# Kernel optimization log

Measured on AMD Instinct MI355X. Metric: run time of the kernel, lower is better.

Reference implementation:

```python
import jax, jax.numpy as jnp
import numpy as np

N, DIN, D, K, H, N_ITERS = 16384, 256, 1024, 64, 2048, 3
THRESH = 0.3
EPS = 1e-8


def layernorm(x):
    mu = jnp.mean(x, axis=-1, keepdims=True)
    var = jnp.var(x, axis=-1, keepdims=True)
    return (x - mu) * jax.lax.rsqrt(var + 1e-5)


def setup_inputs() -> dict:
    key = jax.random.key(0)
    ks = jax.random.split(key, 20)
    s = 0.02
    return {
        "detections_t": jax.random.normal(ks[0], (N, DIN), jnp.float32),
        "detections_t1": jax.random.normal(ks[1], (N, DIN), jnp.float32),
        "W_enc": s * jax.random.normal(ks[2], (DIN, D), jnp.float32),
        "b_enc": jnp.zeros((D,), jnp.float32),
        "Wq": s * jax.random.normal(ks[3], (D, D), jnp.float32),
        "bq": jnp.zeros((D,), jnp.float32),
        "Wk": s * jax.random.normal(ks[4], (D, D), jnp.float32),
        "bk": jnp.zeros((D,), jnp.float32),
        "Wv": s * jax.random.normal(ks[5], (D, D), jnp.float32),
        "bv": jnp.zeros((D,), jnp.float32),
        "Wi": s * jax.random.normal(ks[6], (3 * D, D), jnp.float32),  # GRU input weights
        "Wh": s * jax.random.normal(ks[7], (3 * D, D), jnp.float32),  # GRU hidden weights
        "bi": jnp.zeros((3 * D,), jnp.float32),
        "bh": jnp.zeros((3 * D,), jnp.float32),
        "W1": s * jax.random.normal(ks[8], (D, H), jnp.float32),
        "b1": jnp.zeros((H,), jnp.float32),
        "W2": s * jax.random.normal(ks[9], (H, D), jnp.float32),
        "b2": jnp.zeros((D,), jnp.float32),
        "slots_mu": s * jax.random.normal(ks[10], (1, D), jnp.float32),
        "init_noise": jax.random.normal(ks[11], (K, D), jnp.float32) * s,
    }


def _gru(u, h, Wi, Wh, bi, bh):
    gi = u @ Wi.T + bi          # [K, 3D]
    gh = h @ Wh.T + bh
    ir, iz, inn = jnp.split(gi, 3, axis=-1)
    hr, hz, hn = jnp.split(gh, 3, axis=-1)
    r = jax.nn.sigmoid(ir + hr)
    z = jax.nn.sigmoid(iz + hz)
    n = jnp.tanh(inn + r * hn)
    return (1.0 - z) * n + z * h


def _process_frame(dets, prev_slots, p):
    x = layernorm(dets @ p["W_enc"] + p["b_enc"])          # [N, D]
    k = x @ p["Wk"] + p["bk"]                               # [N, D]
    v = x @ p["Wv"] + p["bv"]                               # [N, D]
    slots = prev_slots if prev_slots is not None else p["slots_mu"] + p["init_noise"]
    scale = D ** -0.5
    for _ in range(N_ITERS):
        slots_prev = slots
        q = layernorm(slots) @ p["Wq"] + p["bq"]            # [K, D]
        dots = (q @ k.T) * scale                             # [K, N]
        attn = jax.nn.softmax(dots, axis=0)                  # slots compete per detection
        attn = attn / (jnp.sum(attn, axis=-1, keepdims=True) + EPS)
        updates = attn @ v                                   # [K, D]
        slots = _gru(updates, slots_prev, p["Wi"], p["Wh"], p["bi"], p["bh"])
        slots = slots + (jax.nn.relu(layernorm(slots) @ p["W1"] + p["b1"]) @ p["W2"] + p["b2"])
    return slots


def _slot_similarity(a, b):
    an = a / (jnp.linalg.norm(a, axis=-1, keepdims=True) + EPS)
    bn = b / (jnp.linalg.norm(b, axis=-1, keepdims=True) + EPS)
    return an @ bn.T                                         # [K, K]


def _greedy_match(sim):
    max_sims = jnp.max(sim, axis=1)
    max_idxs = jnp.argmax(sim, axis=1)
    order = jnp.argsort(-max_sims)
    def step(carry, idx):
        matches, used = carry
        j = max_idxs[idx]
        ok = jnp.logical_and(~used[j], max_sims[idx] > THRESH)
        matches = matches.at[idx].set(jnp.where(ok, j, matches[idx]))
        used = used.at[j].set(used[j] | ok)
        return (matches, used), None
    init = (jnp.full((K,), -1, jnp.int32), jnp.zeros((K,), jnp.bool_))
    (matches, _), _ = jax.lax.scan(step, init, order)
    return matches


def reference(detections_t, detections_t1, W_enc, b_enc, Wq, bq, Wk, bk, Wv, bv,
              Wi, Wh, bi, bh, W1, b1, W2, b2, slots_mu, init_noise):
    p = dict(W_enc=W_enc, b_enc=b_enc, Wq=Wq, bq=bq, Wk=Wk, bk=bk, Wv=Wv, bv=bv,
             Wi=Wi, Wh=Wh, bi=bi, bh=bh, W1=W1, b1=b1, W2=W2, b2=b2,
             slots_mu=slots_mu, init_noise=init_noise)
    prev_slots = _process_frame(detections_t, None, p)
    curr_slots = _process_frame(detections_t1, prev_slots, p)
    sim = _slot_similarity(prev_slots, curr_slots)
    matches = _greedy_match(sim)
    return matches, sim
```

## Files before the change

kernel.cpp:

```cpp
#include <hip/hip_runtime.h>
#include <hip/hip_bf16.h>
#include <type_traits>

typedef __hip_bfloat16 bf16;
typedef __attribute__((ext_vector_type(8))) short s16x8;
typedef __attribute__((ext_vector_type(4))) float f32x4;

#define N_DET 16384
#define DIN   256
#define DD    1024
#define KSLOT 64
#define HH    2048
#define TD    3072

__device__ __forceinline__ float b2f(bf16 x){ return __bfloat162float(x); }
__device__ __forceinline__ bf16  f2b(float x){ return __float2bfloat16(x); }
__device__ __forceinline__ float bits2f(short u){ return __uint_as_float(((unsigned)(unsigned short)u) << 16); }

__device__ __forceinline__ void gload_lds16(const void* g, void* l) {
  __builtin_amdgcn_global_load_lds(
      (const __attribute__((address_space(1))) unsigned int*)g,
      (__attribute__((address_space(3))) unsigned int*)l, 16, 0, 0);
}

__device__ __forceinline__ void big_compute(bf16* As, bf16* Bs,
    const bf16* __restrict__ Ap, const bf16* __restrict__ Bp, int K, f32x4 acc[4][4])
{
  const int tid = threadIdx.x;
  const int lane = tid & 63, wave = tid >> 6;
  const int wr = wave >> 1, wc = wave & 1;
  const int l15 = lane & 15, h = lane >> 4;
  const int rr = tid >> 3;
  const int qs = ((tid & 7) ^ (rr & 7)) * 8;

#pragma unroll
  for (int m = 0; m < 4; ++m)
#pragma unroll
    for (int n = 0; n < 4; ++n) acc[m][n] = {0.f, 0.f, 0.f, 0.f};

  for (int k0 = 0; k0 < K; k0 += 64) {
    __syncthreads();
#pragma unroll
    for (int g = 0; g < 4; ++g)
      gload_lds16(Ap + (size_t)(g * 32 + rr) * K + k0 + qs,
                  As + ((size_t)g * 256 + wave * 64) * 8);
#pragma unroll
    for (int g = 0; g < 4; ++g)
      gload_lds16(Bp + (size_t)(g * 32 + rr) * K + k0 + qs,
                  Bs + ((size_t)g * 256 + wave * 64) * 8);
    __syncthreads();

#pragma unroll
    for (int ks = 0; ks < 2; ++ks) {
      s16x8 af[4], bfr[4];
#pragma unroll
      for (int m = 0; m < 4; ++m) {
        int row = wr * 64 + m * 16 + l15;
        af[m] = *(const s16x8*)&As[row * 64 + (((ks * 4 + h) ^ (l15 & 7)) * 8)];
      }
#pragma unroll
      for (int n = 0; n < 4; ++n) {
        int row = wc * 64 + n * 16 + l15;
        bfr[n] = *(const s16x8*)&Bs[row * 64 + (((ks * 4 + h) ^ (l15 & 7)) * 8)];
      }
#pragma unroll
      for (int m = 0; m < 4; ++m)
#pragma unroll
        for (int n = 0; n < 4; ++n)
          acc[m][n] = __builtin_amdgcn_mfma_f32_16x16x32_bf16(af[m], bfr[n], acc[m][n], 0, 0, 0);
    }
  }
}

__device__ __forceinline__ void big_epilogue(int bm, int bn,
    const float* __restrict__ bias, bf16* __restrict__ C, int N, f32x4 acc[4][4])
{
  const int lane = threadIdx.x & 63, wave = threadIdx.x >> 6;
  const int wr = wave >> 1, wc = wave & 1;
#pragma unroll
  for (int m = 0; m < 4; ++m)
#pragma unroll
    for (int n = 0; n < 4; ++n) {
      int col = bn + wc * 64 + n * 16 + (lane & 15);
      float bv = bias ? bias[col] : 0.f;
#pragma unroll
      for (int j = 0; j < 4; ++j) {
        int row = bm + wr * 64 + m * 16 + (lane >> 4) * 4 + j;
        C[(size_t)row * N + col] = f2b(acc[m][n][j] + bv);
      }
    }
}

__device__ __forceinline__ void big_gemm_body(int wg, int nct,
    const bf16* __restrict__ A, const bf16* __restrict__ Bt,
    const float* __restrict__ bias, bf16* __restrict__ C, int N, int K,
    bf16* As, bf16* Bs)
{
  const int bn = (wg % nct) * 128;
  const int bm = (wg / nct) * 128;
  f32x4 acc[4][4];
  big_compute(As, Bs, A + (size_t)bm * K, Bt + (size_t)bn * K, K, acc);
  big_epilogue(bm, bn, bias, C, N, acc);
}

__global__ __launch_bounds__(256) void gemm_enc(
    const float* __restrict__ A, const bf16* __restrict__ Bt,
    const float* __restrict__ bias, bf16* __restrict__ C, int M, int N, int K)
{
  const int nct = N >> 7;
  const int chunk = gridDim.x >> 3;
  const int wg = (blockIdx.x & 7) * chunk + (blockIdx.x >> 3);
  const int bn = (wg % nct) * 128;
  const int bm = (wg / nct) * 128;

  __shared__ bf16 As[2 * 128 * 64];
  __shared__ bf16 Bs[2 * 128 * 64];
  const int tid = threadIdx.x;
  const int lane = tid & 63, wave = tid >> 6;
  const int l15 = lane & 15, h = lane >> 4;
  const int wr = wave >> 1, wc = wave & 1;
  const int rr = tid >> 3;
  const int qs = ((tid & 7) ^ (rr & 7)) * 8;

  f32x4 acc[4][4];
#pragma unroll
  for (int m = 0; m < 4; ++m)
#pragma unroll
    for (int n = 0; n < 4; ++n) acc[m][n] = {0.f, 0.f, 0.f, 0.f};

  for (int k0 = 0; k0 < K; k0 += 128) {
    __syncthreads();
#pragma unroll
    for (int half = 0; half < 2; ++half) {
#pragma unroll
      for (int g = 0; g < 4; ++g) {
        const float* src = A + (size_t)(bm + g * 32 + rr) * K + k0 + half * 64 + qs;
        float4 f0 = *(const float4*)src;
        float4 f1 = *(const float4*)(src + 4);
        bf16 pk[8] = {f2b(f0.x), f2b(f0.y), f2b(f0.z), f2b(f0.w),
                      f2b(f1.x), f2b(f1.y), f2b(f1.z), f2b(f1.w)};
        *(s16x8*)&As[half * 8192 + g * 2048 + tid * 8] = *(const s16x8*)pk;
      }
#pragma unroll
      for (int g = 0; g < 4; ++g)
        gload_lds16(Bt + (size_t)(bn + g * 32 + rr) * K + k0 + half * 64 + qs,
                    Bs + (size_t)half * 8192 + ((size_t)g * 256 + wave * 64) * 8);
    }
    __syncthreads();

#pragma unroll
    for (int half = 0; half < 2; ++half)
#pragma unroll
      for (int ks = 0; ks < 2; ++ks) {
        s16x8 af[4], bfr[4];
#pragma unroll
        for (int m = 0; m < 4; ++m) {
          int row = wr * 64 + m * 16 + l15;
          af[m] = *(const s16x8*)&As[half * 8192 + row * 64 + (((ks * 4 + h) ^ (l15 & 7)) * 8)];
        }
#pragma unroll
        for (int n = 0; n < 4; ++n) {
          int row = wc * 64 + n * 16 + l15;
          bfr[n] = *(const s16x8*)&Bs[half * 8192 + row * 64 + (((ks * 4 + h) ^ (l15 & 7)) * 8)];
        }
#pragma unroll
        for (int m = 0; m < 4; ++m)
#pragma unroll
          for (int n = 0; n < 4; ++n)
            acc[m][n] = __builtin_amdgcn_mfma_f32_16x16x32_bf16(af[m], bfr[n], acc[m][n], 0, 0, 0);
      }
  }
  big_epilogue(bm, bn, bias, C, N, acc);
}

__global__ __launch_bounds__(256) void gemm_setup_pair(
    const bf16* __restrict__ Wi_b, const bf16* __restrict__ Wv_bf, bf16* __restrict__ Wvit,
    const bf16* __restrict__ Wk_bf, const bf16* __restrict__ Wq_bf, bf16* __restrict__ Wqk_t)
{
  __shared__ bf16 As[128 * 64];
  __shared__ bf16 Bs[128 * 64];
  if (blockIdx.x < 192) {
    int bid = blockIdx.x;
    int wg = (bid & 7) * 24 + (bid >> 3);
    big_gemm_body(wg, 8, Wi_b, Wv_bf, nullptr, Wvit, DD, DD, As, Bs);
  } else {
    int bid = blockIdx.x - 192;
    int wg = (bid & 7) * 8 + (bid >> 3);
    big_gemm_body(wg, 8, Wk_bf, Wq_bf, nullptr, Wqk_t, DD, DD, As, Bs);
  }
}

__device__ __forceinline__ void skinny_compute(bf16* As, bf16* Bs,
    const bf16* __restrict__ A, const bf16* __restrict__ Bt,
    int K, int Kc, int n0, int kb0, f32x4 acc[4])
{
  const int tid = threadIdx.x;
  const int lane = tid & 63, wave = tid >> 6;
  const int rem = wave * 64 + lane;
  const int r = rem >> 2, q = rem & 3;
  const int l15 = lane & 15, h = lane >> 4;

#pragma unroll
  for (int m = 0; m < 4; ++m) acc[m] = {0.f, 0.f, 0.f, 0.f};

  for (int kb = kb0; kb < kb0 + Kc; kb += 256) {
    __syncthreads();
#pragma unroll
    for (int half = 0; half < 2; ++half) {
#pragma unroll
      for (int g = 0; g < 4; ++g)
        gload_lds16(A + (size_t)r * K + kb + half * 128 + g * 32 + q * 8,
                    As + (size_t)half * 8192 + ((size_t)g * 256 + wave * 64) * 8);
#pragma unroll
      for (int g = 0; g < 4; ++g)
        gload_lds16(Bt + (size_t)(n0 + r) * K + kb + half * 128 + g * 32 + q * 8,
                    Bs + (size_t)half * 8192 + ((size_t)g * 256 + wave * 64) * 8);
    }
    __syncthreads();

#pragma unroll
    for (int half = 0; half < 2; ++half)
#pragma unroll
      for (int ks = 0; ks < 4; ++ks) {
        s16x8 bfr = *(const s16x8*)&Bs[half * 8192 + (ks * 64 + wave * 16 + l15) * 32 + h * 8];
#pragma unroll
        for (int m = 0; m < 4; ++m) {
          s16x8 af = *(const s16x8*)&As[half * 8192 + (ks * 64 + m * 16 + l15) * 32 + h * 8];
          acc[m] = __builtin_amdgcn_mfma_f32_16x16x32_bf16(af, bfr, acc[m], 0, 0, 0);
        }
      }
  }
}

template<int EPI>
__global__ __launch_bounds__(256) void gemm_skinny_e(
    const bf16* __restrict__ A, const bf16* __restrict__ Bt,
    float* __restrict__ pbuf, bf16* __restrict__ outb,
    const float* __restrict__ bias, int N, int K, int Kc)
{
  __shared__ bf16 As[2 * 4 * 64 * 32];
  __shared__ bf16 Bs[2 * 4 * 64 * 32];
  f32x4 acc[4];
  skinny_compute(As, Bs, A, Bt, K, Kc, blockIdx.x * 64, blockIdx.y * Kc, acc);

  const int lane = threadIdx.x & 63, wave = threadIdx.x >> 6;
  const int l15 = lane & 15, h = lane >> 4;
#pragma unroll
  for (int m = 0; m < 4; ++m)
#pragma unroll
    for (int j = 0; j < 4; ++j) {
      int row = m * 16 + h * 4 + j;
      int col = blockIdx.x * 64 + wave * 16 + l15;
      if (EPI == 0) {
        pbuf[((size_t)(blockIdx.y * 64) + row) * N + col] = acc[m][j];
      } else {
        float v = acc[m][j] + bias[col];
        if (EPI == 2) v = fmaxf(v, 0.f);
        outb[(size_t)row * N + col] = f2b(v);
      }
    }
}

__global__ __launch_bounds__(256) void gemm_skinny_dual(
    const bf16* __restrict__ A0, const bf16* __restrict__ A1,
    const bf16* __restrict__ B0, const bf16* __restrict__ B1,
    float* __restrict__ p0, float* __restrict__ p1, int N, int K, int Kc)
{
  __shared__ bf16 As[2 * 4 * 64 * 32];
  __shared__ bf16 Bs[2 * 4 * 64 * 32];
  const bf16* A = blockIdx.z ? A1 : A0;
  const bf16* B = blockIdx.z ? B1 : B0;
  float* p = blockIdx.z ? p1 : p0;

  f32x4 acc[4];
  skinny_compute(As, Bs, A, B, K, Kc, blockIdx.x * 64, blockIdx.y * Kc, acc);

  const int lane = threadIdx.x & 63, wave = threadIdx.x >> 6;
  const int l15 = lane & 15, h = lane >> 4;
#pragma unroll
  for (int m = 0; m < 4; ++m)
#pragma unroll
    for (int j = 0; j < 4; ++j) {
      int row = m * 16 + h * 4 + j;
      int col = blockIdx.x * 64 + wave * 16 + l15;
      p[((size_t)(blockIdx.y * 64) + row) * N + col] = acc[m][j];
    }
}

__device__ __forceinline__ void block_ln_store(float v[4], float s, float sq,
    bf16* __restrict__ out, int row,
    const float* __restrict__ wqbk, float* __restrict__ cbuf, float* __restrict__ colsum)
{
  for (int o = 32; o > 0; o >>= 1) { s += __shfl_down(s, o, 64); sq += __shfl_down(sq, o, 64); }
  __shared__ float ls[4], lq[4];
  int w = threadIdx.x >> 6;
  if ((threadIdx.x & 63) == 0) { ls[w] = s; lq[w] = sq; }
  __syncthreads();
  s  = ls[0] + ls[1] + ls[2] + ls[3];
  sq = lq[0] + lq[1] + lq[2] + lq[3];
  float mu = s * (1.f / DD);
  float var = sq * (1.f / DD) - mu * mu;
  float rstd = rsqrtf(var + 1e-5f);
#pragma unroll
  for (int j = 0; j < 4; j++)
    out[(size_t)row * DD + threadIdx.x + j * 256] = f2b((v[j] - mu) * rstd);
  if (wqbk) {
    float dot = 0.f;
#pragma unroll
    for (int j = 0; j < 4; j++) dot += (v[j] - mu) * rstd * wqbk[threadIdx.x + j * 256];
    for (int o = 32; o > 0; o >>= 1) dot += __shfl_down(dot, o, 64);
    __syncthreads();
    if ((threadIdx.x & 63) == 0) ls[w] = dot;
    __syncthreads();
    if (threadIdx.x == 0) { cbuf[row] = ls[0] + ls[1] + ls[2] + ls[3]; colsum[row] = 0.f; }
  }
}

__global__ __launch_bounds__(256) void gru_reduce_ln(const float* __restrict__ pA,
    const float* __restrict__ pB, const float* __restrict__ bvi,
    const float* __restrict__ bh, float* __restrict__ slots, bf16* __restrict__ lnb)
{
  int s = blockIdx.x, t = threadIdx.x;
  float v[4], sum = 0.f, sq = 0.f;
#pragma unroll
  for (int j = 0; j < 4; ++j) {
    int d = t + j * 256;
    const float* a = pA + (size_t)s * TD;
    const float* b = pB + (size_t)s * TD;
    float ir = bvi[d] + a[d], iz = bvi[1024 + d] + a[1024 + d], in_ = bvi[2048 + d] + a[2048 + d];
    float hr = bh[d] + b[d], hz = bh[1024 + d] + b[1024 + d], hnn = bh[2048 + d] + b[2048 + d];
    float r = 1.f / (1.f + expf(-(ir + hr)));
    float z = 1.f / (1.f + expf(-(iz + hz)));
    float nn = tanhf(in_ + r * hnn);
    float h = slots[(size_t)s * DD + d];
    float hv = (1.f - z) * nn + z * h;
    slots[(size_t)s * DD + d] = hv;
    v[j] = hv; sum += hv; sq += hv * hv;
  }
  block_ln_store(v, sum, sq, lnb, s, nullptr, nullptr, nullptr);
}

template<int SK>
__global__ __launch_bounds__(256) void mlp2_reduce_ln(const float* __restrict__ pbuf,
    const float* __restrict__ bias, float* __restrict__ slots,
    bf16* __restrict__ slotspb, bf16* __restrict__ lnb,
    const float* __restrict__ wqbk, float* __restrict__ cbuf, float* __restrict__ colsum,
    float* __restrict__ prevs)
{
  int s = blockIdx.x, t = threadIdx.x;
  float v[4], sum = 0.f, sq = 0.f;
#pragma unroll
  for (int j = 0; j < 4; ++j) {
    int d = t + j * 256;
    float x = bias[d] + slots[(size_t)s * DD + d];
#pragma unroll
    for (int sk = 0; sk < SK; ++sk) x += pbuf[(size_t)(sk * 64 + s) * DD + d];
    slots[(size_t)s * DD + d] = x;
    slotspb[(size_t)s * DD + d] = f2b(x);
    if (prevs) prevs[(size_t)s * DD + d] = x;
    v[j] = x; sum += x; sq += x * x;
  }
  block_ln_store(v, sum, sq, lnb, s, wqbk, cbuf, colsum);
}

__global__ __launch_bounds__(256) void slots_init_ln(const float* __restrict__ mu,
    const float* __restrict__ noise, float* __restrict__ slots,
    bf16* __restrict__ slotspb, bf16* __restrict__ lnb,
    const float* __restrict__ wqbk, float* __restrict__ cbuf, float* __restrict__ colsum)
{
  int s = blockIdx.x, t = threadIdx.x;
  float v[4], sum = 0.f, sq = 0.f;
#pragma unroll
  for (int j = 0; j < 4; ++j) {
    int d = t + j * 256;
    float x = mu[d] + noise[(size_t)s * DD + d];
    slots[(size_t)s * DD + d] = x;
    slotspb[(size_t)s * DD + d] = f2b(x);
    v[j] = x; sum += x; sq += x * x;
  }
  block_ln_store(v, sum, sq, lnb, s, wqbk, cbuf, colsum);
}

__global__ __launch_bounds__(256) void qk_softmax(const bf16* __restrict__ qkb,
    const bf16* __restrict__ x, const float* __restrict__ cbuf,
    bf16* __restrict__ attn, float* __restrict__ colsum)
{
  __shared__ bf16 Qs[4 * 64 * 64];
  __shared__ bf16 Ks[4 * 64 * 64];
  __shared__ float cs[64], cl[64];
  const int t = threadIdx.x, lane = t & 63, wave = t >> 6;
  const int n0 = blockIdx.x * 64;
  const int l15 = lane & 15, h = lane >> 4;
  if (t < 64) { cs[t] = 0.f; cl[t] = cbuf[t]; }

  f32x4 acc[4];
#pragma unroll
  for (int m = 0; m < 4; ++m) acc[m] = {0.f, 0.f, 0.f, 0.f};

  for (int k0 = 0; k0 < DD; k0 += 256) {
    __syncthreads();
#pragma unroll
    for (int half = 0; half < 4; ++half) {
#pragma unroll
      for (int c = 0; c < 2; ++c) {
        int i = c * 256 + t;
        int r = i >> 3, q8 = i & 7;
        gload_lds16(qkb + (size_t)r * DD + k0 + half * 64 + q8 * 8,
                    Qs + (size_t)half * 4096 + ((size_t)c * 256 + wave * 64) * 8);
      }
#pragma unroll
      for (int c = 0; c < 2; ++c) {
        int i = c * 256 + t;
        int r = i >> 3, q8 = i & 7;
        gload_lds16(x + (size_t)(n0 + r) * DD + k0 + half * 64 + q8 * 8,
                    Ks + (size_t)half * 4096 + ((size_t)c * 256 + wave * 64) * 8);
      }
    }
    __syncthreads();

#pragma unroll
    for (int half = 0; half < 4; ++half)
#pragma unroll
      for (int ks = 0; ks < 2; ++ks) {
        s16x8 bfr = *(const s16x8*)&Ks[half * 4096 + (wave * 16 + l15) * 64 + ks * 32 + h * 8];
#pragma unroll
        for (int m = 0; m < 4; ++m) {
          s16x8 af = *(const s16x8*)&Qs[half * 4096 + (m * 16 + l15) * 64 + ks * 32 + h * 8];
          acc[m] = __builtin_amdgcn_mfma_f32_16x16x32_bf16(af, bfr, acc[m], 0, 0, 0);
        }
      }
  }

  float e[4][4];
  float cmax = -1e30f;
#pragma unroll
  for (int m = 0; m < 4; ++m)
#pragma unroll
    for (int j = 0; j < 4; ++j) {
      e[m][j] = (acc[m][j] + cl[m * 16 + h * 4 + j]) * 0.03125f;
      cmax = fmaxf(cmax, e[m][j]);
    }
  cmax = fmaxf(cmax, __shfl_xor(cmax, 16, 64));
  cmax = fmaxf(cmax, __shfl_xor(cmax, 32, 64));
  float ssum = 0.f;
#pragma unroll
  for (int m = 0; m < 4; ++m)
#pragma unroll
    for (int j = 0; j < 4; ++j) { e[m][j] = expf(e[m][j] - cmax); ssum += e[m][j]; }
  ssum += __shfl_xor(ssum, 16, 64);
  ssum += __shfl_xor(ssum, 32, 64);
  float inv = 1.f / ssum;
  __syncthreads();

  const int n = n0 + wave * 16 + l15;
#pragma unroll
  for (int m = 0; m < 4; ++m)
#pragma unroll
    for (int j = 0; j < 4; ++j) {
      float a = e[m][j] * inv;
      int s = m * 16 + h * 4 + j;
      attn[(size_t)s * N_DET + n] = f2b(a);
      float v = a;
      v += __shfl_xor(v, 1, 64);
      v += __shfl_xor(v, 2, 64);
      v += __shfl_xor(v, 4, 64);
      v += __shfl_xor(v, 8, 64);
      if (l15 == 0) atomicAdd(&cs[s], v);
    }
  __syncthreads();
  if (t < 64) atomicAdd(&colsum[t], cs[t]);
}

template<int SK>
__global__ __launch_bounds__(256) void updates_reduce2(const float* __restrict__ pbuf,
    const float* __restrict__ colsum, bf16* __restrict__ tb)
{
  int s = blockIdx.y, d = blockIdx.x * 256 + threadIdx.x;
  float v = 0.f;
#pragma unroll
  for (int sk = 0; sk < SK; ++sk) v += pbuf[(size_t)(sk * 64 + s) * DD + d];
  tb[(size_t)s * DD + d] = f2b(v / (colsum[s] + 1e-8f));
}

__global__ __launch_bounds__(256) void setup_all(
    const float* __restrict__ W_enc, const float* __restrict__ W1, const float* __restrict__ W2,
    bf16* __restrict__ Wenc_t, bf16* __restrict__ W1_t, bf16* __restrict__ W2_t,
    const float* __restrict__ Wh, const float* __restrict__ Wi,
    const float* __restrict__ Wv, const float* __restrict__ Wq, const float* __restrict__ Wk,
    bf16* __restrict__ oWh, bf16* __restrict__ oWi, bf16* __restrict__ oWv,
    bf16* __restrict__ oWq, bf16* __restrict__ oWk,
    const float* __restrict__ bv, const float* __restrict__ bk, const float* __restrict__ bq,
    const float* __restrict__ bi,
    float* __restrict__ bvi, float* __restrict__ wqbk, float* __restrict__ bqk)
{
  __shared__ float t[32][33];
  int b = blockIdx.x;
  if (b < 4352) {
    const float* W; bf16* Wt; int K, N, bx, by;
    if (b < 256)       { W = W_enc; Wt = Wenc_t; K = DIN;  N = DD; bx = b & 31;  by = b >> 5; }
    else if (b < 2304) { int r = b - 256;  W = W1; Wt = W1_t; K = DD;  N = HH; bx = r & 63; by = r >> 6; }
    else               { int r = b - 2304; W = W2; Wt = W2_t; K = HH;  N = DD; bx = r & 31; by = r >> 5; }
    int n0 = bx * 32, k0 = by * 32;
    int tx = threadIdx.x & 31, ty = threadIdx.x >> 5;
    for (int r = ty; r < 32; r += 8)
      t[r][tx] = W[(size_t)(k0 + r) * N + n0 + tx];
    __syncthreads();
    for (int r = ty; r < 32; r += 8)
      Wt[(size_t)(n0 + r) * K + k0 + tx] = f2b(t[tx][r]);
  } else if (b < 13568) {
    int cb = b - 4352;
    const float* src; bf16* dst; int base;
    if      (cb < 3072) { src = Wh; dst = oWh; base = cb; }
    else if (cb < 6144) { src = Wi; dst = oWi; base = cb - 3072; }
    else if (cb < 7168) { src = Wv; dst = oWv; base = cb - 6144; }
    else if (cb < 8192) { src = Wq; dst = oWq; base = cb - 7168; }
    else                { src = Wk; dst = oWk; base = cb - 8192; }
    int i = (base * 256 + threadIdx.x) * 4;
    float4 v = *(const float4*)(src + i);
    bf16 o[4] = {f2b(v.x), f2b(v.y), f2b(v.z), f2b(v.w)};
    *(ushort4*)(dst + i) = *(const ushort4*)o;
  } else {
    int row = (b - 13568) * 4 + (threadIdx.x >> 6);
    int lane = threadIdx.x & 63;
    const float* w; const float* vec; float s0; float* out; int idx;
    if (row < 3072)      { idx = row;        w = Wi + (size_t)idx * DD; vec = bv; s0 = bi[idx]; out = bvi; }
    else if (row < 4096) { idx = row - 3072; w = Wq + (size_t)idx * DD; vec = bk; s0 = 0.f;     out = wqbk; }
    else                 { idx = row - 4096; w = Wk + (size_t)idx * DD; vec = bq; s0 = 0.f;     out = bqk; }
    float s = 0.f;
#pragma unroll
    for (int c = 0; c < 4; ++c) {
      float4 wv = *(const float4*)(w + c * 256 + lane * 4);
      float4 bb = *(const float4*)(vec + c * 256 + lane * 4);
      s += wv.x * bb.x + wv.y * bb.y + wv.z * bb.z + wv.w * bb.w;
    }
    for (int o = 32; o > 0; o >>= 1) s += __shfl_down(s, o, 64);
    if (lane == 0) out[idx] = s0 + s;
  }
}

__global__ __launch_bounds__(256) void ln_stats(const bf16* __restrict__ x_pre,
                                                float2* __restrict__ stats)
{
  int row = blockIdx.x * 4 + (threadIdx.x >> 6);
  int lane = threadIdx.x & 63;
  const bf16* p = x_pre + (size_t)row * DD + lane * 16;
  s16x8 v0 = *(const s16x8*)p;
  s16x8 v1 = *(const s16x8*)(p + 8);
  float s = 0.f, sq = 0.f;
#pragma unroll
  for (int j = 0; j < 8; ++j) {
    float a = bits2f(v0[j]), b = bits2f(v1[j]);
    s += a + b; sq += a * a + b * b;
  }
  for (int o = 32; o > 0; o >>= 1) { s += __shfl_down(s, o, 64); sq += __shfl_down(sq, o, 64); }
  if (lane == 0) {
    float mu = s * (1.f / DD);
    float var = sq * (1.f / DD) - mu * mu;
    stats[row] = make_float2(mu, rsqrtf(var + 1e-5f));
  }
}

__global__ __launch_bounds__(256) void norm_transpose(const bf16* __restrict__ x_pre,
    const float2* __restrict__ stats, bf16* __restrict__ x, bf16* __restrict__ xT)
{
  __shared__ bf16 t[64][70];
  int n0 = blockIdx.x * 64, d0 = blockIdx.y * 64;
  int r = threadIdx.x >> 2, c = (threadIdx.x & 3) * 16;
  float2 st = stats[n0 + r];
  s16x8 v0 = *(const s16x8*)&x_pre[(size_t)(n0 + r) * DD + d0 + c];
  s16x8 v1 = *(const s16x8*)&x_pre[(size_t)(n0 + r) * DD + d0 + c + 8];
  bf16 o16[16];
#pragma unroll
  for (int j = 0; j < 8; ++j) {
    o16[j]     = f2b((bits2f(v0[j]) - st.x) * st.y);
    o16[8 + j] = f2b((bits2f(v1[j]) - st.x) * st.y);
  }
  *(s16x8*)&x[(size_t)(n0 + r) * DD + d0 + c]     = *(const s16x8*)&o16[0];
  *(s16x8*)&x[(size_t)(n0 + r) * DD + d0 + c + 8] = *(const s16x8*)&o16[8];
#pragma unroll
  for (int j = 0; j < 16; ++j) t[c + j][r] = o16[j];
  __syncthreads();
  bf16 o[16];
#pragma unroll
  for (int j = 0; j < 16; ++j) o[j] = t[r][c + j];
  *(s16x8*)&xT[(size_t)(d0 + r) * N_DET + n0 + c]     = *(const s16x8*)&o[0];
  *(s16x8*)&xT[(size_t)(d0 + r) * N_DET + n0 + c + 8] = *(const s16x8*)&o[8];
}

__global__ __launch_bounds__(256) void sim_fused(const float* __restrict__ prevs,
    const float* __restrict__ slots, float* __restrict__ simout)
{
  __shared__ float ar[1024];
  __shared__ float lq[4];
  int i = blockIdx.x, t = threadIdx.x;
  float v[4], sq = 0.f;
#pragma unroll
  for (int j = 0; j < 4; j++) { v[j] = prevs[(size_t)i * DD + t + j * 256]; sq += v[j] * v[j]; }
  for (int o = 32; o > 0; o >>= 1) sq += __shfl_down(sq, o, 64);
  int w = t >> 6;
  if ((t & 63) == 0) lq[w] = sq;
  __syncthreads();
  sq = lq[0] + lq[1] + lq[2] + lq[3];
  float sc = 1.f / (sqrtf(sq) + 1e-8f);
#pragma unroll
  for (int j = 0; j < 4; j++) ar[t + j * 256] = v[j] * sc;
  __syncthreads();

  int jr = t >> 2, g = t & 3;
  float dot = 0.f, ss = 0.f;
  for (int d = g; d < 1024; d += 4) {
    float b = slots[(size_t)jr * DD + d];
    dot += ar[d] * b; ss += b * b;
  }
  dot += __shfl_xor(dot, 1, 64); ss += __shfl_xor(ss, 1, 64);
  dot += __shfl_xor(dot, 2, 64); ss += __shfl_xor(ss, 2, 64);
  if (g == 0) simout[i * 64 + jr] = dot / (sqrtf(ss) + 1e-8f);
}

__global__ void match_kernel(const float* __restrict__ sim, float* __restrict__ outm)
{
  __shared__ float m[64];
  __shared__ int idx[64];
  __shared__ int order[64];
  __shared__ int used[64];
  int i = threadIdx.x;
  float best = -1e30f; int bj = 0;
  for (int j = 0; j < 64; j++) {
    float v = sim[i * 64 + j];
    if (v > best) { best = v; bj = j; }
  }
  m[i] = best; idx[i] = bj; used[i] = 0;
  __syncthreads();
  int cnt = 0;
  for (int j = 0; j < 64; j++) {
    float mj = m[j];
    if (mj > best || (mj == best && j < i)) cnt++;
  }
  order[cnt] = i;
  __syncthreads();
  if (i == 0) {
    for (int r = 0; r < 64; r++) {
      int ii = order[r];
      int j = idx[ii];
      bool ok = (!used[j]) && (m[ii] > 0.3f);
      outm[ii] = ok ? (float)j : -1.0f;
      if (ok) used[j] = 1;
    }
  }
}

static constexpr size_t OFF_XPRE = 0;
static constexpr size_t OFF_ATT  = 0;
static constexpr size_t OFF_PA   = (size_t)4  << 20;
static constexpr size_t OFF_P0   = (size_t)8  << 20;
static constexpr size_t OFF_P1   = (size_t)10 << 20;
static constexpr size_t OFF_WET  = (size_t)32 << 20;
static constexpr size_t OFF_WQKT = OFF_WET + ((size_t)512 << 10);
static constexpr size_t OFF_W1T  = OFF_WQKT + ((size_t)2 << 20);
static constexpr size_t OFF_W2T  = OFF_W1T + ((size_t)4 << 20);
static constexpr size_t OFF_WHB  = OFF_W2T + ((size_t)4 << 20);
static constexpr size_t OFF_WVIT = OFF_WHB + ((size_t)6 << 20);
static constexpr size_t OFF_X    = (size_t)60 << 20;
static constexpr size_t OFF_WIB  = OFF_X;
static constexpr size_t OFF_WVB  = OFF_X + ((size_t)6 << 20);
static constexpr size_t OFF_WQB  = OFF_X + ((size_t)8 << 20);
static constexpr size_t OFF_WKB  = OFF_X + ((size_t)10 << 20);
static constexpr size_t OFF_XT   = OFF_X + ((size_t)32 << 20);
static constexpr size_t OFF_SM   = OFF_XT + ((size_t)32 << 20);
static constexpr size_t OFF_SL   = OFF_SM;
static constexpr size_t OFF_SLPB = OFF_SL  + 262144;
static constexpr size_t OFF_LNB  = OFF_SLPB + 131072;
static constexpr size_t OFF_QKB  = OFF_LNB + 131072;
static constexpr size_t OFF_TB   = OFF_QKB + 131072;
static constexpr size_t OFF_HIDB = OFF_TB  + 131072;
static constexpr size_t OFF_PRV  = OFF_HIDB + 262144;
static constexpr size_t OFF_CS   = OFF_PRV + 262144;
static constexpr size_t OFF_BVI  = OFF_CS  + 4096;
static constexpr size_t OFF_WQBK = OFF_BVI + 16384;
static constexpr size_t OFF_BQK  = OFF_WQBK + 4096;
static constexpr size_t OFF_STAT = OFF_BQK + 4096;

extern "C" void kernel_launch(void* const* d_in, const int* in_sizes, int n_in,
                              void* d_out, int out_size, void* d_ws, size_t ws_size,
                              hipStream_t stream)
{
  (void)in_sizes; (void)n_in; (void)out_size; (void)ws_size;
  const float* dets_t   = (const float*)d_in[0];
  const float* dets_t1  = (const float*)d_in[1];
  const float* W_enc    = (const float*)d_in[2];
  const float* b_enc    = (const float*)d_in[3];
  const float* Wq       = (const float*)d_in[4];
  const float* bq       = (const float*)d_in[5];
  const float* Wk       = (const float*)d_in[6];
  const float* bk       = (const float*)d_in[7];
  const float* Wv       = (const float*)d_in[8];
  const float* bv       = (const float*)d_in[9];
  const float* Wi       = (const float*)d_in[10];
  const float* Wh       = (const float*)d_in[11];
  const float* bi       = (const float*)d_in[12];
  const float* bh       = (const float*)d_in[13];
  const float* W1       = (const float*)d_in[14];
  const float* b1       = (const float*)d_in[15];
  const float* W2       = (const float*)d_in[16];
  const float* b2       = (const float*)d_in[17];
  const float* slots_mu = (const float*)d_in[18];
  const float* init_noise = (const float*)d_in[19];

  char* ws = (char*)d_ws;
  bf16*  x_pre  = (bf16*)(ws + OFF_XPRE);
  bf16*  attn   = (bf16*)(ws + OFF_ATT);
  float* pA     = (float*)(ws + OFF_PA);
  float* p0     = (float*)(ws + OFF_P0);
  float* p1     = (float*)(ws + OFF_P1);
  bf16*  Wenc_t = (bf16*)(ws + OFF_WET);
  bf16*  Wqk_t  = (bf16*)(ws + OFF_WQKT);
  bf16*  W1_t   = (bf16*)(ws + OFF_W1T);
  bf16*  W2_t   = (bf16*)(ws + OFF_W2T);
  bf16*  Wh_b   = (bf16*)(ws + OFF_WHB);
  bf16*  Wvit   = (bf16*)(ws + OFF_WVIT);
  bf16*  Wi_b   = (bf16*)(ws + OFF_WIB);
  bf16*  Wv_bf  = (bf16*)(ws + OFF_WVB);
  bf16*  Wq_bf  = (bf16*)(ws + OFF_WQB);
  bf16*  Wk_bf  = (bf16*)(ws + OFF_WKB);
  bf16*  x      = (bf16*)(ws + OFF_X);
  bf16*  xT     = (bf16*)(ws + OFF_XT);
  float* slots  = (float*)(ws + OFF_SL);
  bf16*  slotspb= (bf16*)(ws + OFF_SLPB);
  bf16*  lnb    = (bf16*)(ws + OFF_LNB);
  bf16*  qkb    = (bf16*)(ws + OFF_QKB);
  bf16*  tb     = (bf16*)(ws + OFF_TB);
  bf16*  hidb   = (bf16*)(ws + OFF_HIDB);
  float* prevs  = (float*)(ws + OFF_PRV);
  float* colsum = (float*)(ws + OFF_CS);
  float* cbuf   = colsum + 64;
  float* bvi    = (float*)(ws + OFF_BVI);
  float* wqbk   = (float*)(ws + OFF_WQBK);
  float* bqk    = (float*)(ws + OFF_BQK);
  float2* stats = (float2*)(ws + OFF_STAT);

  setup_all<<<14848, 256, 0, stream>>>(W_enc, W1, W2, Wenc_t, W1_t, W2_t,
                                       Wh, Wi, Wv, Wq, Wk, Wh_b, Wi_b, Wv_bf, Wq_bf, Wk_bf,
                                       bv, bk, bq, bi, bvi, wqbk, bqk);
  gemm_setup_pair<<<256, 256, 0, stream>>>(Wi_b, Wv_bf, Wvit, Wk_bf, Wq_bf, Wqk_t);

  auto frame = [&](const float* dets, bool first) {
    gemm_enc<<<1024, 256, 0, stream>>>(dets, Wenc_t, b_enc, x_pre, N_DET, DD, DIN);
    ln_stats<<<4096, 256, 0, stream>>>(x_pre, stats);
    norm_transpose<<<dim3(256, 16), 256, 0, stream>>>(x_pre, stats, x, xT);
    if (first) slots_init_ln<<<64, 256, 0, stream>>>(slots_mu, init_noise, slots, slotspb, lnb, wqbk, cbuf, colsum);
    for (int it = 0; it < 3; ++it) {
      gemm_skinny_e<1><<<dim3(16, 1), 256, 0, stream>>>(lnb, Wqk_t, nullptr, qkb, bqk, DD, DD, DD);
      qk_softmax<<<256, 256, 0, stream>>>(qkb, x, cbuf, attn, colsum);
      gemm_skinny_e<0><<<dim3(16, 16), 256, 0, stream>>>(attn, xT, pA, nullptr, nullptr, DD, N_DET, 1024);
      updates_reduce2<16><<<dim3(4, 64), 256, 0, stream>>>(pA, colsum, tb);
      gemm_skinny_dual<<<dim3(48, 1, 2), 256, 0, stream>>>(tb, slotspb, Wvit, Wh_b, p0, p1, TD, DD, DD);
      gru_reduce_ln<<<64, 256, 0, stream>>>(p0, p1, bvi, bh, slots, lnb);
      gemm_skinny_e<2><<<dim3(32, 1), 256, 0, stream>>>(lnb, W1_t, nullptr, hidb, b1, HH, DD, DD);
      gemm_skinny_e<0><<<dim3(16, 2), 256, 0, stream>>>(hidb, W2_t, pA, nullptr, nullptr, DD, HH, 1024);
      mlp2_reduce_ln<2><<<64, 256, 0, stream>>>(pA, b2, slots, slotspb, lnb, wqbk, cbuf, colsum,
                                                (first && it == 2) ? prevs : nullptr);
    }
  };

  frame(dets_t, true);
  frame(dets_t1, false);

  float* outf = (float*)d_out;
  sim_fused<<<KSLOT, 256, 0, stream>>>(prevs, slots, outf + 64);
  match_kernel<<<1, 64, 0, stream>>>(outf + 64, outf);
}
```

Measured before the change: 638.8 us.

## Fuse per-iteration slot update chain into one persistent kernel with grid barriers

Replaces the seven small per-iteration launches (update reduce, dual GRU GEMM, GRU+LN, MLP1, MLP2, residual+LN, next QK projection) with a single 96-block kernel that separates the stages with an atomic-counter grid barrier. The QK projection moves to the end of each iteration, and the barrier counter is reset in setup. The goal is to remove kernel launch and drain overhead on the latency-bound slot chain. The risk is that the spin barrier only works if all 96 blocks are co-resident, and idle blocks in the narrow stages waste occupancy. The encoder GEMM is also changed from double-width staging to a single 64-wide K tile per sync.

```diff
diff --git a/kernel.cpp b/kernel.cpp
--- a/kernel.cpp
+++ b/kernel.cpp
@@ -12,6 +12,7 @@
 #define KSLOT 64
 #define HH    2048
 #define TD    3072
+#define CHAIN_BLOCKS 96
 
 __device__ __forceinline__ float b2f(bf16 x){ return __bfloat162float(x); }
 __device__ __forceinline__ bf16  f2b(float x){ return __float2bfloat16(x); }
@@ -21,6 +22,17 @@
   __builtin_amdgcn_global_load_lds(
       (const __attribute__((address_space(1))) unsigned int*)g,
       (__attribute__((address_space(3))) unsigned int*)l, 16, 0, 0);
+}
+
+__device__ __forceinline__ void gsync(int* bar, int n) {
+  __syncthreads();
+  if (threadIdx.x == 0) {
+    __threadfence();
+    atomicAdd(bar, 1);
+    while (atomicAdd(bar, 0) < n * CHAIN_BLOCKS) { __builtin_amdgcn_s_sleep(1); }
+    __threadfence();
+  }
+  __syncthreads();
 }
 
 __device__ __forceinline__ void big_compute(bf16* As, bf16* Bs,
@@ -113,8 +125,8 @@
   const int bn = (wg % nct) * 128;
   const int bm = (wg / nct) * 128;
 
-  __shared__ bf16 As[2 * 128 * 64];
-  __shared__ bf16 Bs[2 * 128 * 64];
+  __shared__ bf16 As[128 * 64];
+  __shared__ bf16 Bs[128 * 64];
   const int tid = threadIdx.x;
   const int lane = tid & 63, wave = tid >> 6;
   const int l15 = lane & 15, h = lane >> 4;
@@ -128,47 +140,42 @@
 #pragma unroll
     for (int n = 0; n < 4; ++n) acc[m][n] = {0.f, 0.f, 0.f, 0.f};
 
-  for (int k0 = 0; k0 < K; k0 += 128) {
-    __syncthreads();
-#pragma unroll
-    for (int half = 0; half < 2; ++half) {
-#pragma unroll
-      for (int g = 0; g < 4; ++g) {
-        const float* src = A + (size_t)(bm + g * 32 + rr) * K + k0 + half * 64 + qs;
-        float4 f0 = *(const float4*)src;
-        float4 f1 = *(const float4*)(src + 4);
-        bf16 pk[8] = {f2b(f0.x), f2b(f0.y), f2b(f0.z), f2b(f0.w),
-                      f2b(f1.x), f2b(f1.y), f2b(f1.z), f2b(f1.w)};
-        *(s16x8*)&As[half * 8192 + g * 2048 + tid * 8] = *(const s16x8*)pk;
-      }
-#pragma unroll
-      for (int g = 0; g < 4; ++g)
-        gload_lds16(Bt + (size_t)(bn + g * 32 + rr) * K + k0 + half * 64 + qs,
-                    Bs + (size_t)half * 8192 + ((size_t)g * 256 + wave * 64) * 8);
-    }
-    __syncthreads();
-
-#pragma unroll
-    for (int half = 0; half < 2; ++half)
-#pragma unroll
-      for (int ks = 0; ks < 2; ++ks) {
-        s16x8 af[4], bfr[4];
-#pragma unroll
-        for (int m = 0; m < 4; ++m) {
-          int row = wr * 64 + m * 16 + l15;
-          af[m] = *(const s16x8*)&As[half * 8192 + row * 64 + (((ks * 4 + h) ^ (l15 & 7)) * 8)];
-        }
-#pragma unroll
-        for (int n = 0; n < 4; ++n) {
-          int row = wc * 64 + n * 16 + l15;
-          bfr[n] = *(const s16x8*)&Bs[half * 8192 + row * 64 + (((ks * 4 + h) ^ (l15 & 7)) * 8)];
-        }
-#pragma unroll
-        for (int m = 0; m < 4; ++m)
-#pragma unroll
-          for (int n = 0; n < 4; ++n)
-            acc[m][n] = __builtin_amdgcn_mfma_f32_16x16x32_bf16(af[m], bfr[n], acc[m][n], 0, 0, 0);
-      }
+  for (int k0 = 0; k0 < K; k0 += 64) {
+    __syncthreads();
+#pragma unroll
+    for (int g = 0; g < 4; ++g) {
+      const float* src = A + (size_t)(bm + g * 32 + rr) * K + k0 + qs;
+      float4 f0 = *(const float4*)src;
+      float4 f1 = *(const float4*)(src + 4);
+      bf16 pk[8] = {f2b(f0.x), f2b(f0.y), f2b(f0.z), f2b(f0.w),
+                    f2b(f1.x), f2b(f1.y), f2b(f1.z), f2b(f1.w)};
+      *(s16x8*)&As[g * 2048 + tid * 8] = *(const s16x8*)pk;
+    }
+#pragma unroll
+    for (int g = 0; g < 4; ++g)
+      gload_lds16(Bt + (size_t)(bn + g * 32 + rr) * K + k0 + qs,
+                  Bs + ((size_t)g * 256 + wave * 64) * 8);
+    __syncthreads();
+
+#pragma unroll
+    for (int ks = 0; ks < 2; ++ks) {
+      s16x8 af[4], bfr[4];
+#pragma unroll
+      for (int m = 0; m < 4; ++m) {
+        int row = wr * 64 + m * 16 + l15;
+        af[m] = *(const s16x8*)&As[row * 64 + (((ks * 4 + h) ^ (l15 & 7)) * 8)];
+      }
+#pragma unroll
+      for (int n = 0; n < 4; ++n) {
+        int row = wc * 64 + n * 16 + l15;
+        bfr[n] = *(const s16x8*)&Bs[row * 64 + (((ks * 4 + h) ^ (l15 & 7)) * 8)];
+      }
+#pragma unroll
+      for (int m = 0; m < 4; ++m)
+#pragma unroll
+        for (int n = 0; n < 4; ++n)
+          acc[m][n] = __builtin_amdgcn_mfma_f32_16x16x32_bf16(af[m], bfr[n], acc[m][n], 0, 0, 0);
+    }
   }
   big_epilogue(bm, bn, bias, C, N, acc);
 }
@@ -255,35 +262,8 @@
         pbuf[((size_t)(blockIdx.y * 64) + row) * N + col] = acc[m][j];
       } else {
         float v = acc[m][j] + bias[col];
-        if (EPI == 2) v = fmaxf(v, 0.f);
         outb[(size_t)row * N + col] = f2b(v);
       }
-    }
-}
-
-__global__ __launch_bounds__(256) void gemm_skinny_dual(
-    const bf16* __restrict__ A0, const bf16* __restrict__ A1,
-    const bf16* __restrict__ B0, const bf16* __restrict__ B1,
-    float* __restrict__ p0, float* __restrict__ p1, int N, int K, int Kc)
-{
-  __shared__ bf16 As[2 * 4 * 64 * 32];
-  __shared__ bf16 Bs[2 * 4 * 64 * 32];
-  const bf16* A = blockIdx.z ? A1 : A0;
-  const bf16* B = blockIdx.z ? B1 : B0;
-  float* p = blockIdx.z ? p1 : p0;
-
-  f32x4 acc[4];
-  skinny_compute(As, Bs, A, B, K, Kc, blockIdx.x * 64, blockIdx.y * Kc, acc);
-
-  const int lane = threadIdx.x & 63, wave = threadIdx.x >> 6;
-  const int l15 = lane & 15, h = lane >> 4;
-#pragma unroll
-  for (int m = 0; m < 4; ++m)
-#pragma unroll
-    for (int j = 0; j < 4; ++j) {
-      int row = m * 16 + h * 4 + j;
-      int col = blockIdx.x * 64 + wave * 16 + l15;
-      p[((size_t)(blockIdx.y * 64) + row) * N + col] = acc[m][j];
     }
 }
 
@@ -314,53 +294,6 @@
     __syncthreads();
     if (threadIdx.x == 0) { cbuf[row] = ls[0] + ls[1] + ls[2] + ls[3]; colsum[row] = 0.f; }
   }
-}
-
-__global__ __launch_bounds__(256) void gru_reduce_ln(const float* __restrict__ pA,
-    const float* __restrict__ pB, const float* __restrict__ bvi,
-    const float* __restrict__ bh, float* __restrict__ slots, bf16* __restrict__ lnb)
-{
-  int s = blockIdx.x, t = threadIdx.x;
-  float v[4], sum = 0.f, sq = 0.f;
-#pragma unroll
-  for (int j = 0; j < 4; ++j) {
-    int d = t + j * 256;
-    const float* a = pA + (size_t)s * TD;
-    const float* b = pB + (size_t)s * TD;
-    float ir = bvi[d] + a[d], iz = bvi[1024 + d] + a[1024 + d], in_ = bvi[2048 + d] + a[2048 + d];
-    float hr = bh[d] + b[d], hz = bh[1024 + d] + b[1024 + d], hnn = bh[2048 + d] + b[2048 + d];
-    float r = 1.f / (1.f + expf(-(ir + hr)));
-    float z = 1.f / (1.f + expf(-(iz + hz)));
-    float nn = tanhf(in_ + r * hnn);
-    float h = slots[(size_t)s * DD + d];
-    float hv = (1.f - z) * nn + z * h;
-    slots[(size_t)s * DD + d] = hv;
-    v[j] = hv; sum += hv; sq += hv * hv;
-  }
-  block_ln_store(v, sum, sq, lnb, s, nullptr, nullptr, nullptr);
-}
-
-template<int SK>
-__global__ __launch_bounds__(256) void mlp2_reduce_ln(const float* __restrict__ pbuf,
-    const float* __restrict__ bias, float* __restrict__ slots,
-    bf16* __restrict__ slotspb, bf16* __restrict__ lnb,
-    const float* __restrict__ wqbk, float* __restrict__ cbuf, float* __restrict__ colsum,
-    float* __restrict__ prevs)
-{
-  int s = blockIdx.x, t = threadIdx.x;
-  float v[4], sum = 0.f, sq = 0.f;
-#pragma unroll
-  for (int j = 0; j < 4; ++j) {
-    int d = t + j * 256;
-    float x = bias[d] + slots[(size_t)s * DD + d];
-#pragma unroll
-    for (int sk = 0; sk < SK; ++sk) x += pbuf[(size_t)(sk * 64 + s) * DD + d];
-    slots[(size_t)s * DD + d] = x;
-    slotspb[(size_t)s * DD + d] = f2b(x);
-    if (prevs) prevs[(size_t)s * DD + d] = x;
-    v[j] = x; sum += x; sq += x * x;
-  }
-  block_ln_store(v, sum, sq, lnb, s, wqbk, cbuf, colsum);
 }
 
 __global__ __launch_bounds__(256) void slots_init_ln(const float* __restrict__ mu,
@@ -379,6 +312,136 @@
     v[j] = x; sum += x; sq += x * x;
   }
   block_ln_store(v, sum, sq, lnb, s, wqbk, cbuf, colsum);
+}
+
+__global__ __launch_bounds__(256) void iter_chain(
+    const float* __restrict__ pU, float* __restrict__ colsum, float* __restrict__ cbuf,
+    bf16* __restrict__ tb,
+    const bf16* __restrict__ Wvit, const bf16* __restrict__ Wh_b,
+    float* __restrict__ p0, float* __restrict__ p1,
+    const float* __restrict__ bvi, const float* __restrict__ bh,
+    float* __restrict__ slots, bf16* __restrict__ lnb,
+    const bf16* __restrict__ W1_t, const float* __restrict__ b1, bf16* __restrict__ hidb,
+    const bf16* __restrict__ W2_t, float* __restrict__ pW2,
+    const float* __restrict__ b2, bf16* __restrict__ slotspb,
+    const float* __restrict__ wqbk,
+    const bf16* __restrict__ Wqk_t, const float* __restrict__ bqk, bf16* __restrict__ qkb,
+    float* __restrict__ prevs, int save_prevs,
+    int* __restrict__ bar, int barBase)
+{
+  __shared__ bf16 As[2 * 4 * 64 * 32];
+  __shared__ bf16 Bs[2 * 4 * 64 * 32];
+  const int bid = blockIdx.x, tid = threadIdx.x;
+  const int lane = tid & 63, wave = tid >> 6;
+  const int l15 = lane & 15, h = lane >> 4;
+  int bno = barBase;
+
+  for (int idx = bid * 256 + tid; idx < KSLOT * DD; idx += CHAIN_BLOCKS * 256) {
+    int s = idx >> 10, d = idx & 1023;
+    float v = 0.f;
+#pragma unroll
+    for (int sk = 0; sk < 16; ++sk) v += pU[(size_t)(sk * 64 + s) * DD + d];
+    tb[(size_t)s * DD + d] = f2b(v / (colsum[s] + 1e-8f));
+  }
+  gsync(bar, ++bno);
+
+  {
+    int z = bid >= 48, bx = z ? bid - 48 : bid;
+    f32x4 acc[4];
+    skinny_compute(As, Bs, z ? slotspb : tb, z ? Wh_b : Wvit, DD, DD, bx * 64, 0, acc);
+    float* p = z ? p1 : p0;
+#pragma unroll
+    for (int m = 0; m < 4; ++m)
+#pragma unroll
+      for (int j = 0; j < 4; ++j) {
+        int row = m * 16 + h * 4 + j;
+        int col = bx * 64 + wave * 16 + l15;
+        p[(size_t)row * TD + col] = acc[m][j];
+      }
+  }
+  gsync(bar, ++bno);
+
+  if (bid < 64) {
+    int s = bid;
+    float v[4], sum = 0.f, sq = 0.f;
+#pragma unroll
+    for (int j = 0; j < 4; ++j) {
+      int d = tid + j * 256;
+      const float* a = p0 + (size_t)s * TD;
+      const float* b = p1 + (size_t)s * TD;
+      float ir = bvi[d] + a[d], iz = bvi[1024 + d] + a[1024 + d], in_ = bvi[2048 + d] + a[2048 + d];
+      float hr = bh[d] + b[d], hz = bh[1024 + d] + b[1024 + d], hnn = bh[2048 + d] + b[2048 + d];
+      float r = 1.f / (1.f + expf(-(ir + hr)));
+      float z = 1.f / (1.f + expf(-(iz + hz)));
+      float nn = tanhf(in_ + r * hnn);
+      float hld = slots[(size_t)s * DD + d];
+      float hv = (1.f - z) * nn + z * hld;
+      slots[(size_t)s * DD + d] = hv;
+      v[j] = hv; sum += hv; sq += hv * hv;
+    }
+    block_ln_store(v, sum, sq, lnb, s, nullptr, nullptr, nullptr);
+  }
+  gsync(bar, ++bno);
+
+  if (bid < 32) {
+    f32x4 acc[4];
+    skinny_compute(As, Bs, lnb, W1_t, DD, DD, bid * 64, 0, acc);
+#pragma unroll
+    for (int m = 0; m < 4; ++m)
+#pragma unroll
+      for (int j = 0; j < 4; ++j) {
+        int row = m * 16 + h * 4 + j;
+        int col = bid * 64 + wave * 16 + l15;
+        hidb[(size_t)row * HH + col] = f2b(fmaxf(acc[m][j] + b1[col], 0.f));
+      }
+  }
+  gsync(bar, ++bno);
+
+  if (bid < 32) {
+    int bx = bid & 15, by = bid >> 4;
+    f32x4 acc[4];
+    skinny_compute(As, Bs, hidb, W2_t, HH, 1024, bx * 64, by * 1024, acc);
+#pragma unroll
+    for (int m = 0; m < 4; ++m)
+#pragma unroll
+      for (int j = 0; j < 4; ++j) {
+        int row = m * 16 + h * 4 + j;
+        int col = bx * 64 + wave * 16 + l15;
+        pW2[((size_t)(by * 64) + row) * DD + col] = acc[m][j];
+      }
+  }
+  gsync(bar, ++bno);
+
+  if (bid < 64) {
+    int s = bid;
+    float v[4], sum = 0.f, sq = 0.f;
+#pragma unroll
+    for (int j = 0; j < 4; ++j) {
+      int d = tid + j * 256;
+      float x = b2[d] + slots[(size_t)s * DD + d];
+#pragma unroll
+      for (int sk = 0; sk < 2; ++sk) x += pW2[(size_t)(sk * 64 + s) * DD + d];
+      slots[(size_t)s * DD + d] = x;
+      slotspb[(size_t)s * DD + d] = f2b(x);
+      if (save_prevs) prevs[(size_t)s * DD + d] = x;
+      v[j] = x; sum += x; sq += x * x;
+    }
+    block_ln_store(v, sum, sq, lnb, s, wqbk, cbuf, colsum);
+  }
+  gsync(bar, ++bno);
+
+  if (bid < 16) {
+    f32x4 acc[4];
+    skinny_compute(As, Bs, lnb, Wqk_t, DD, DD, bid * 64, 0, acc);
+#pragma unroll
+    for (int m = 0; m < 4; ++m)
+#pragma unroll
+      for (int j = 0; j < 4; ++j) {
+        int row = m * 16 + h * 4 + j;
+        int col = bid * 64 + wave * 16 + l15;
+        qkb[(size_t)row * DD + col] = f2b(acc[m][j] + bqk[col]);
+      }
+  }
 }
 
 __global__ __launch_bounds__(256) void qk_softmax(const bf16* __restrict__ qkb,
@@ -471,17 +534,6 @@
   if (t < 64) atomicAdd(&colsum[t], cs[t]);
 }
 
-template<int SK>
-__global__ __launch_bounds__(256) void updates_reduce2(const float* __restrict__ pbuf,
-    const float* __restrict__ colsum, bf16* __restrict__ tb)
-{
-  int s = blockIdx.y, d = blockIdx.x * 256 + threadIdx.x;
-  float v = 0.f;
-#pragma unroll
-  for (int sk = 0; sk < SK; ++sk) v += pbuf[(size_t)(sk * 64 + s) * DD + d];
-  tb[(size_t)s * DD + d] = f2b(v / (colsum[s] + 1e-8f));
-}
-
 __global__ __launch_bounds__(256) void setup_all(
     const float* __restrict__ W_enc, const float* __restrict__ W1, const float* __restrict__ W2,
     bf16* __restrict__ Wenc_t, bf16* __restrict__ W1_t, bf16* __restrict__ W2_t,
@@ -491,10 +543,12 @@
     bf16* __restrict__ oWq, bf16* __restrict__ oWk,
     const float* __restrict__ bv, const float* __restrict__ bk, const float* __restrict__ bq,
     const float* __restrict__ bi,
-    float* __restrict__ bvi, float* __restrict__ wqbk, float* __restrict__ bqk)
+    float* __restrict__ bvi, float* __restrict__ wqbk, float* __restrict__ bqk,
+    int* __restrict__ bar)
 {
   __shared__ float t[32][33];
   int b = blockIdx.x;
+  if (b == 0 && threadIdx.x == 0) *bar = 0;
   if (b < 4352) {
     const float* W; bf16* Wt; int K, N, bx, by;
     if (b < 256)       { W = W_enc; Wt = Wenc_t; K = DIN;  N = DD; bx = b & 31;  by = b >> 5; }
@@ -733,6 +787,7 @@
   float* prevs  = (float*)(ws + OFF_PRV);
   float* colsum = (float*)(ws + OFF_CS);
   float* cbuf   = colsum + 64;
+  int*   bar    = (int*)(colsum + 128);
   float* bvi    = (float*)(ws + OFF_BVI);
   float* wqbk   = (float*)(ws + OFF_WQBK);
   float* bqk    = (float*)(ws + OFF_BQK);
@@ -740,25 +795,27 @@
 
   setup_all<<<14848, 256, 0, stream>>>(W_enc, W1, W2, Wenc_t, W1_t, W2_t,
                                        Wh, Wi, Wv, Wq, Wk, Wh_b, Wi_b, Wv_bf, Wq_bf, Wk_bf,
-                                       bv, bk, bq, bi, bvi, wqbk, bqk);
+                                       bv, bk, bq, bi, bvi, wqbk, bqk, bar);
   gemm_setup_pair<<<256, 256, 0, stream>>>(Wi_b, Wv_bf, Wvit, Wk_bf, Wq_bf, Wqk_t);
 
+  int coopj = 0;
   auto frame = [&](const float* dets, bool first) {
     gemm_enc<<<1024, 256, 0, stream>>>(dets, Wenc_t, b_enc, x_pre, N_DET, DD, DIN);
     ln_stats<<<4096, 256, 0, stream>>>(x_pre, stats);
     norm_transpose<<<dim3(256, 16), 256, 0, stream>>>(x_pre, stats, x, xT);
-    if (first) slots_init_ln<<<64, 256, 0, stream>>>(slots_mu, init_noise, slots, slotspb, lnb, wqbk, cbuf, colsum);
+    if (first) {
+      slots_init_ln<<<64, 256, 0, stream>>>(slots_mu, init_noise, slots, slotspb, lnb, wqbk, cbuf, colsum);
+      gemm_skinny_e<1><<<dim3(16, 1), 256, 0, stream>>>(lnb, Wqk_t, nullptr, qkb, bqk, DD, DD, DD);
+    }
     for (int it = 0; it < 3; ++it) {
-      gemm_skinny_e<1><<<dim3(16, 1), 256, 0, stream>>>(lnb, Wqk_t, nullptr, qkb, bqk, DD, DD, DD);
       qk_softmax<<<256, 256, 0, stream>>>(qkb, x, cbuf, attn, colsum);
       gemm_skinny_e<0><<<dim3(16, 16), 256, 0, stream>>>(attn, xT, pA, nullptr, nullptr, DD, N_DET, 1024);
-      updates_reduce2<16><<<dim3(4, 64), 256, 0, stream>>>(pA, colsum, tb);
-      gemm_skinny_dual<<<dim3(48, 1, 2), 256, 0, stream>>>(tb, slotspb, Wvit, Wh_b, p0, p1, TD, DD, DD);
-      gru_reduce_ln<<<64, 256, 0, stream>>>(p0, p1, bvi, bh, slots, lnb);
-      gemm_skinny_e<2><<<dim3(32, 1), 256, 0, stream>>>(lnb, W1_t, nullptr, hidb, b1, HH, DD, DD);
-      gemm_skinny_e<0><<<dim3(16, 2), 256, 0, stream>>>(hidb, W2_t, pA, nullptr, nullptr, DD, HH, 1024);
-      mlp2_reduce_ln<2><<<64, 256, 0, stream>>>(pA, b2, slots, slotspb, lnb, wqbk, cbuf, colsum,
-                                                (first && it == 2) ? prevs : nullptr);
+      int save = (first && it == 2) ? 1 : 0;
+      iter_chain<<<CHAIN_BLOCKS, 256, 0, stream>>>(pA, colsum, cbuf, tb, Wvit, Wh_b, p0, p1,
+                                                   bvi, bh, slots, lnb, W1_t, b1, hidb,
+                                                   W2_t, pA, b2, slotspb, wqbk,
+                                                   Wqk_t, bqk, qkb, prevs, save, bar, coopj * 6);
+      ++coopj;
     }
   };
 
```

Result: slower. 843.8 us (+32.1%).
